# Kernel tuning notes

Measured on AMD Instinct MI355X. Metric: run time of the kernel, lower is better.

The kernel has to match this reference:

```python
import jax, jax.numpy as jnp
import numpy as np

B, C, H, W = 16, 256, 224, 224

def border_mask(h, w, dtype=jnp.float32):
    # Bresenham lines along the 4 edges of the rectangle == 1-pixel border ring.
    ys = jnp.arange(h)
    xs = jnp.arange(w)
    on_border = (ys[:, None] == 0) | (ys[:, None] == h - 1) | (xs[None, :] == 0) | (xs[None, :] == w - 1)
    return on_border.astype(dtype)  # [H, W]

def setup_inputs() -> dict:
    key = jax.random.key(0)
    k1, k2 = jax.random.split(key)
    x = jax.random.normal(k1, (B, C, H, W), dtype=jnp.float32)
    conv_w = jax.random.normal(k2, (1, C, 1, 1), dtype=jnp.float32) * (1.0 / np.sqrt(C))
    conv_b = jnp.zeros((1,), dtype=jnp.float32)
    return {"x": x, "conv_w": conv_w, "conv_b": conv_b}

def reference(x, conv_w, conv_b):
    # 1x1 conv to a single channel: contraction over C.
    w = conv_w[0, :, 0, 0]  # [C]
    att = jnp.einsum('bchw,c->bhw', x, w) + conv_b[0]  # [B,H,W]
    att = jax.nn.sigmoid(att)
    mask = border_mask(x.shape[2], x.shape[3], x.dtype)  # [H,W], identical for all batches
    combined = att * (1.0 + mask)  # [B,H,W]
    return x * combined[:, None, :, :]  # [B,C,H,W]
```

## Files before the change

### kernel.cpp

```cpp
#include <hip/hip_runtime.h>

constexpr int C  = 256;
constexpr int H  = 224;
constexpr int W  = 224;
constexpr int HW = H * W;
constexpr int PIX = 64;
constexpr int THREADS = 256;
constexpr int TILES_PER_B = HW / PIX;
constexpr int BATCH = 16;

__global__ __launch_bounds__(THREADS, 2)
void fused_sigmoid_border_scale(const float* __restrict__ x,
                                const float* __restrict__ wv,
                                const float* __restrict__ bv,
                                float* __restrict__ out)
{
    __shared__ float tile[C * PIX];
    __shared__ float partial[4 * PIX];
    __shared__ float comb[PIX];

    const int t   = threadIdx.x;
    const int blk = blockIdx.x;
    const int b   = blk / TILES_PER_B;
    const int hw0 = (blk - b * TILES_PER_B) * PIX;

    const float* xb = x   + (size_t)b * C * HW + hw0;
    float*       ob = out + (size_t)b * C * HW + hw0;

    const int q  = t & 15;
    const int c0 = t >> 4;

    #pragma unroll
    for (int k = 0; k < 16; ++k) {
        const int c = k * 16 + c0;
        float4 v = *reinterpret_cast<const float4*>(xb + (size_t)c * HW + q * 4);
        *reinterpret_cast<float4*>(&tile[c * PIX + q * 4]) = v;
    }
    __syncthreads();

    {
        const int cg = t >> 6;
        const int p  = t & 63;
        const float* wp = wv + cg * 64;
        const float* tp = tile + (cg * 64) * PIX + p;
        float s = 0.f;
        #pragma unroll
        for (int k = 0; k < 64; ++k)
            s += tp[k * PIX] * wp[k];
        partial[cg * PIX + p] = s;
    }
    __syncthreads();

    if (t < PIX) {
        float s = partial[t] + partial[PIX + t] + partial[2 * PIX + t]
                + partial[3 * PIX + t] + bv[0];
        float att = 1.0f / (1.0f + expf(-s));
        const int hw = hw0 + t;
        const int h  = hw / W;
        const int w  = hw - h * W;
        const bool border = (h == 0) | (h == H - 1) | (w == 0) | (w == W - 1);
        comb[t] = att * (border ? 2.0f : 1.0f);
    }
    __syncthreads();

    const float4 m = *reinterpret_cast<const float4*>(&comb[q * 4]);
    #pragma unroll
    for (int k = 0; k < 16; ++k) {
        const int c = k * 16 + c0;
        float4 v = *reinterpret_cast<const float4*>(&tile[c * PIX + q * 4]);
        v.x *= m.x; v.y *= m.y; v.z *= m.z; v.w *= m.w;
        *reinterpret_cast<float4*>(ob + (size_t)c * HW + q * 4) = v;
    }
}

extern "C" void kernel_launch(void* const* d_in, const int* in_sizes, int n_in,
                              void* d_out, int out_size, void* d_ws, size_t ws_size,
                              hipStream_t stream) {
    const float* x  = (const float*)d_in[0];
    const float* wv = (const float*)d_in[1];
    const float* bv = (const float*)d_in[2];
    float* out = (float*)d_out;

    dim3 grid(BATCH * TILES_PER_B);
    fused_sigmoid_border_scale<<<grid, THREADS, 0, stream>>>(x, wv, bv, out);
}
```

Measured before the change: 330.8 us.

## Keep input tile in registers and reduce via wave shuffles instead of LDS

Result: faster. 314.6 us (-4.9%).

```diff
diff --git a/kernel.cpp b/kernel.cpp
--- a/kernel.cpp
+++ b/kernel.cpp
@@ -9,14 +9,15 @@
 constexpr int TILES_PER_B = HW / PIX;
 constexpr int BATCH = 16;
 
-__global__ __launch_bounds__(THREADS, 2)
+typedef float f32x4 __attribute__((ext_vector_type(4)));
+
+__global__ __launch_bounds__(THREADS, 4)
 void fused_sigmoid_border_scale(const float* __restrict__ x,
                                 const float* __restrict__ wv,
                                 const float* __restrict__ bv,
                                 float* __restrict__ out)
 {
-    __shared__ float tile[C * PIX];
-    __shared__ float partial[4 * PIX];
+    __shared__ f32x4 pw[4][16];
     __shared__ float comb[PIX];
 
     const int t   = threadIdx.x;
@@ -27,34 +28,43 @@
     const float* xb = x   + (size_t)b * C * HW + hw0;
     float*       ob = out + (size_t)b * C * HW + hw0;
 
-    const int q  = t & 15;
-    const int c0 = t >> 4;
+    const int q    = t & 15;
+    const int c0   = t >> 4;
+    const int wave = t >> 6;
 
+    f32x4 v[16];
     #pragma unroll
     for (int k = 0; k < 16; ++k) {
         const int c = k * 16 + c0;
-        float4 v = *reinterpret_cast<const float4*>(xb + (size_t)c * HW + q * 4);
-        *reinterpret_cast<float4*>(&tile[c * PIX + q * 4]) = v;
+        v[k] = __builtin_nontemporal_load(
+            reinterpret_cast<const f32x4*>(xb + (size_t)c * HW + q * 4));
     }
-    __syncthreads();
 
-    {
-        const int cg = t >> 6;
-        const int p  = t & 63;
-        const float* wp = wv + cg * 64;
-        const float* tp = tile + (cg * 64) * PIX + p;
-        float s = 0.f;
-        #pragma unroll
-        for (int k = 0; k < 64; ++k)
-            s += tp[k * PIX] * wp[k];
-        partial[cg * PIX + p] = s;
+    f32x4 acc = (f32x4)(0.f);
+    #pragma unroll
+    for (int k = 0; k < 16; ++k) {
+        const float wk = wv[k * 16 + c0];
+        acc.x = fmaf(v[k].x, wk, acc.x);
+        acc.y = fmaf(v[k].y, wk, acc.y);
+        acc.z = fmaf(v[k].z, wk, acc.z);
+        acc.w = fmaf(v[k].w, wk, acc.w);
     }
+
+    #pragma unroll
+    for (int m = 16; m <= 32; m <<= 1) {
+        acc.x += __shfl_xor(acc.x, m);
+        acc.y += __shfl_xor(acc.y, m);
+        acc.z += __shfl_xor(acc.z, m);
+        acc.w += __shfl_xor(acc.w, m);
+    }
+    if ((t & 63) < 16) pw[wave][q] = acc;
     __syncthreads();
 
     if (t < PIX) {
-        float s = partial[t] + partial[PIX + t] + partial[2 * PIX + t]
-                + partial[3 * PIX + t] + bv[0];
-        float att = 1.0f / (1.0f + expf(-s));
+        const int qq = t >> 2, cc = t & 3;
+        float s = pw[0][qq][cc] + pw[1][qq][cc] + pw[2][qq][cc] + pw[3][qq][cc]
+                + bv[0];
+        const float att = 1.0f / (1.0f + expf(-s));
         const int hw = hw0 + t;
         const int h  = hw / W;
         const int w  = hw - h * W;
@@ -63,13 +73,13 @@
     }
     __syncthreads();
 
-    const float4 m = *reinterpret_cast<const float4*>(&comb[q * 4]);
+    const f32x4 m4 = *reinterpret_cast<const f32x4*>(&comb[q * 4]);
     #pragma unroll
     for (int k = 0; k < 16; ++k) {
         const int c = k * 16 + c0;
-        float4 v = *reinterpret_cast<const float4*>(&tile[c * PIX + q * 4]);
-        v.x *= m.x; v.y *= m.y; v.z *= m.z; v.w *= m.w;
-        *reinterpret_cast<float4*>(ob + (size_t)c * HW + q * 4) = v;
+        f32x4 r = v[k] * m4;
+        __builtin_nontemporal_store(r,
+            reinterpret_cast<f32x4*>(ob + (size_t)c * HW + q * 4));
     }
 }
 
```
